# Performance work log

Hardware: AMD Instinct MI355X
Metric: run time of the kernel (lower is better)

The kernel has to match this reference:

```python
import jax, jax.numpy as jnp
import numpy as np

D_MODEL = 1024
N_HEAD = 16
D_HEAD = 64
BSZ = 2
QLEN = 2048
LOCAL_SIZE = 1000
LN_EPS = 1e-5


def setup_inputs() -> dict:
    key = jax.random.key(0)
    ks = jax.random.split(key, 8)
    z1ss = jax.random.normal(ks[0], (BSZ, D_MODEL, QLEN), jnp.float32)
    pos_emb = jax.random.normal(ks[1], (1, D_MODEL, QLEN), jnp.float32)
    u1ss = jax.random.normal(ks[2], (BSZ, 3 * N_HEAD * D_HEAD, QLEN), jnp.float32) * 0.05
    W_qkv = jax.random.normal(ks[3], (3 * N_HEAD * D_HEAD, D_MODEL), jnp.float32) * 0.02
    W_r = jax.random.normal(ks[4], (N_HEAD * D_HEAD, D_MODEL), jnp.float32) * 0.02
    r_w_bias = jax.random.uniform(ks[5], (N_HEAD, D_HEAD), jnp.float32, -0.05, 0.05)
    r_r_bias = jax.random.uniform(ks[6], (N_HEAD, D_HEAD), jnp.float32, -0.05, 0.05)
    W_o = jax.random.normal(ks[7], (D_MODEL, N_HEAD * D_HEAD), jnp.float32) * 0.02
    b_o = jnp.zeros((D_MODEL,), jnp.float32)
    return dict(z1ss=z1ss, pos_emb=pos_emb, u1ss=u1ss, W_qkv=W_qkv, W_r=W_r,
                r_w_bias=r_w_bias, r_r_bias=r_r_bias, W_o=W_o, b_o=b_o)


def _rel_shift(x):
    # Transformer-XL relative-shift trick: pad one column on the left, reshape,
    # drop first row, reshape back. x: [b, n, qlen, klen]
    b, n, q, k = x.shape
    xp = jnp.pad(x, ((0, 0), (0, 0), (0, 0), (1, 0)))
    return xp.reshape(b, n, k + 1, q)[:, :, 1:, :].reshape(b, n, q, k)


def reference(z1ss, pos_emb, u1ss, W_qkv, W_r, r_w_bias, r_r_bias, W_o, b_o):
    bsz, d_model, qlen = z1ss.shape
    n_head, d_head = r_w_bias.shape
    klen = qlen  # mems=None -> mlen=0
    scale = 1.0 / (d_head ** 0.5)

    # Conv1d(kernel_size=1, bias=False) == per-position linear
    w_heads = jnp.einsum('od,bdq->boq', W_qkv, z1ss) + u1ss        # [b, 3*n*d, q]
    r_head_k = jnp.einsum('od,dq->oq', W_r, pos_emb[0]).reshape(n_head, d_head, klen)

    q_h, k_h, v_h = jnp.split(w_heads, 3, axis=1)
    q_h = q_h.reshape(bsz, n_head, d_head, qlen)
    k_h = k_h.reshape(bsz, n_head, d_head, klen)
    v_h = v_h.reshape(bsz, n_head, d_head, klen)

    AC = jnp.einsum('bndi,bndj->bnij', q_h + r_w_bias[:, :, None], k_h)
    BD = _rel_shift(jnp.einsum('bndi,ndj->bnij', q_h + r_r_bias[:, :, None], r_head_k))
    attn_score = (AC + BD) * scale                                  # [b, n, q, k]

    # causal + local-window mask (mlen=0)
    ones = jnp.ones((qlen, klen), dtype=bool)
    mask = jnp.triu(ones, 1) | jnp.tril(ones, -LOCAL_SIZE)
    attn_score = jnp.where(mask[None, None], -jnp.inf, attn_score)

    attn_prob = jax.nn.softmax(attn_score, axis=-1)
    attn_vec = jnp.einsum('bnij,bndj->bndi', attn_prob, v_h)
    attn_vec = attn_vec.reshape(bsz, n_head * d_head, qlen)

    attn_out = jnp.einsum('od,bdq->boq', W_o, attn_vec) + b_o[None, :, None]

    # post-LN residual: layer_norm over d_model (no affine params)
    x = (attn_out + z1ss).transpose(0, 2, 1)                        # [b, q, d]
    mu = x.mean(-1, keepdims=True)
    var = ((x - mu) ** 2).mean(-1, keepdims=True)
    x = (x - mu) / jnp.sqrt(var + LN_EPS)
    return x.transpose(0, 2, 1)                                     # [b, d, q]
```

## Files before the change

kernel.cpp:

```cpp
#include <hip/hip_runtime.h>
#include <hip/hip_bf16.h>

#define D_MODEL 1024
#define N_HEAD 16
#define BSZ 2
#define QLEN 2048
#define LOCAL_SIZE 1000
#define QKV3 (3 * N_HEAD * 64)

typedef __hip_bfloat16 bf16;
typedef short bf16x8 __attribute__((ext_vector_type(8)));
typedef float f32x4 __attribute__((ext_vector_type(4)));

static __device__ __forceinline__ float b2f(bf16 x) { return __bfloat162float(x); }
static __device__ __forceinline__ float bits2f(unsigned short u) {
    return __uint_as_float(((unsigned int)u) << 16);
}
static __device__ __forceinline__ unsigned short f2bs(float x) {
    __hip_bfloat16 h = __float2bfloat16(x);
    return *(unsigned short*)&h;
}

static __device__ __forceinline__ int rmode(int m, int fl) { return (m == 2) ? fl : m; }
static __device__ __forceinline__ float ldm(const void* p, size_t i, int isf) {
    return isf ? ((const float*)p)[i] : b2f(((const bf16*)p)[i]);
}
static __device__ __forceinline__ float4 ld4(const void* p, size_t i, int isf) {
    if (isf) return ((const float4*)p)[i >> 2];
    ushort4 u = ((const ushort4*)p)[i >> 2];
    float4 f;
    f.x = bits2f(u.x); f.y = bits2f(u.y); f.z = bits2f(u.z); f.w = bits2f(u.w);
    return f;
}
static __device__ __forceinline__ ushort4 cvt4(float4 f) {
    ushort4 u;
    u.x = f2bs(f.x); u.y = f2bs(f.y); u.z = f2bs(f.z); u.w = f2bs(f.w);
    return u;
}

__global__ void detect_kernel(const unsigned short* __restrict__ w, int* __restrict__ flag)
{
    if (threadIdx.x == 0 && blockIdx.x == 0) {
        int good = 0;
        for (int i = 0; i < 256; ++i) {
            float v = bits2f(w[i]);
            if (v == v && fabsf(v) < 8.0f) ++good;
        }
        *flag = (good >= 240) ? 0 : 1;
    }
}

__global__ __launch_bounds__(256)
void transpose_cvt(const void* __restrict__ in, bf16* __restrict__ outp,
                   int rows, int cols, size_t sIn, size_t sOut,
                   const int* __restrict__ flag)
{
    const int fl = *flag;
    const int b  = blockIdx.z;
    const int c0 = blockIdx.x * 32;
    const int r0 = blockIdx.y * 32;
    const int tx = threadIdx.x & 31, ty = threadIdx.x >> 5;
    __shared__ float T[32][33];
#pragma unroll
    for (int r = 0; r < 4; ++r) {
        int rr = r0 + ty + r * 8;
        T[ty + r * 8][tx] = ldm(in, (size_t)b * sIn + (size_t)rr * cols + c0 + tx, fl);
    }
    __syncthreads();
#pragma unroll
    for (int r = 0; r < 4; ++r) {
        int cc = c0 + ty + r * 8;
        outp[(size_t)b * sOut + (size_t)cc * rows + r0 + tx] =
            __float2bfloat16(T[tx][ty + r * 8]);
    }
}

__global__ __launch_bounds__(256)
void gemm_bf16(const void* __restrict__ A, int mA, size_t sAb,
               const void* __restrict__ B, int mB, size_t sBb,
               void* __restrict__ C, int c_is_bf16, size_t sCb,
               const void* __restrict__ addm, int mAdd, size_t sAddb,
               const void* __restrict__ bias, int mBias,
               int M, int N, int K, const int* __restrict__ flag)
{
    const int fl = *flag;
    const int fA = rmode(mA, fl), fB = rmode(mB, fl);
    const int fAdd = rmode(mAdd, fl), fBias = rmode(mBias, fl);

    const int bz = blockIdx.z;
    const int n0 = blockIdx.x * 128;
    const int m0 = blockIdx.y * 128;
    const int tid = threadIdx.x;
    const int wave = tid >> 6, lane = tid & 63;
    const int quad = lane >> 4, l15 = lane & 15;
    const int wm = (wave >> 1) * 64, wn = (wave & 1) * 64;

    __shared__ unsigned short A_s[128][40];
    __shared__ unsigned short B_s[128][40];

    const int r0c = tid >> 2,         c0c = tid & 3;
    const int r1c = (tid + 256) >> 2, c1c = tid & 3;

    const size_t aOff = (size_t)bz * sAb;
    const size_t bOff = (size_t)bz * sBb;
    const bf16*  Ah = (const bf16*)A;
    const float* Af = (const float*)A;
    const bf16*  Bh = (const bf16*)B;
    const float* Bf = (const float*)B;

    uint4 pa[4], pb[4];

#define LOAD_OP(p, fX, Xh, Xf, xOff, R0, C0, R1, C1, base, k0)                          \
    do {                                                                                \
        if (!fX) {                                                                      \
            p[0] = *(const uint4*)(Xh + xOff + (size_t)(base + R0) * K + (k0) + C0 * 8);\
            p[1] = *(const uint4*)(Xh + xOff + (size_t)(base + R1) * K + (k0) + C1 * 8);\
        } else {                                                                        \
            const float* q0 = Xf + xOff + (size_t)(base + R0) * K + (k0) + C0 * 8;      \
            const float* q1 = Xf + xOff + (size_t)(base + R1) * K + (k0) + C1 * 8;      \
            p[0] = *(const uint4*)q0; p[1] = *(const uint4*)(q0 + 4);                   \
            p[2] = *(const uint4*)q1; p[3] = *(const uint4*)(q1 + 4);                   \
        }                                                                               \
    } while (0)

#define WRITE_OP(p, fX, S, R0, C0, R1, C1)                                              \
    do {                                                                                \
        if (!fX) {                                                                      \
            *(uint4*)&S[R0][C0 * 8] = p[0];                                             \
            *(uint4*)&S[R1][C1 * 8] = p[1];                                             \
        } else {                                                                        \
            float4 f0 = *(float4*)&p[0], f1 = *(float4*)&p[1];                          \
            float4 f2 = *(float4*)&p[2], f3 = *(float4*)&p[3];                          \
            *(ushort4*)&S[R0][C0 * 8]     = cvt4(f0);                                   \
            *(ushort4*)&S[R0][C0 * 8 + 4] = cvt4(f1);                                   \
            *(ushort4*)&S[R1][C1 * 8]     = cvt4(f2);                                   \
            *(ushort4*)&S[R1][C1 * 8 + 4] = cvt4(f3);                                   \
        }                                                                               \
    } while (0)

    f32x4 acc[4][4];
#pragma unroll
    for (int i = 0; i < 4; ++i)
#pragma unroll
        for (int j = 0; j < 4; ++j) acc[i][j] = (f32x4){0.f, 0.f, 0.f, 0.f};

    LOAD_OP(pa, fA, Ah, Af, aOff, r0c, c0c, r1c, c1c, m0, 0);
    LOAD_OP(pb, fB, Bh, Bf, bOff, r0c, c0c, r1c, c1c, n0, 0);

    for (int k0 = 0; k0 < K; k0 += 32) {
        WRITE_OP(pa, fA, A_s, r0c, c0c, r1c, c1c);
        WRITE_OP(pb, fB, B_s, r0c, c0c, r1c, c1c);
        __syncthreads();

        const int kn = k0 + 32;
        if (kn < K) {
            LOAD_OP(pa, fA, Ah, Af, aOff, r0c, c0c, r1c, c1c, m0, kn);
            LOAD_OP(pb, fB, Bh, Bf, bOff, r0c, c0c, r1c, c1c, n0, kn);
        }

        bf16x8 a[4], bb[4];
#pragma unroll
        for (int i = 0; i < 4; ++i)
            a[i] = *(const bf16x8*)&A_s[wm + i * 16 + l15][quad * 8];
#pragma unroll
        for (int j = 0; j < 4; ++j)
            bb[j] = *(const bf16x8*)&B_s[wn + j * 16 + l15][quad * 8];
#pragma unroll
        for (int i = 0; i < 4; ++i)
#pragma unroll
            for (int j = 0; j < 4; ++j)
                acc[i][j] = __builtin_amdgcn_mfma_f32_16x16x32_bf16(a[i], bb[j], acc[i][j], 0, 0, 0);
        __syncthreads();
    }
#undef LOAD_OP
#undef WRITE_OP

    const size_t cb = (size_t)bz * sCb;
#pragma unroll
    for (int i = 0; i < 4; ++i) {
#pragma unroll
        for (int j = 0; j < 4; ++j) {
            int n = n0 + wn + j * 16 + l15;
#pragma unroll
            for (int r = 0; r < 4; ++r) {
                int m = m0 + wm + i * 16 + quad * 4 + r;
                float v = acc[i][j][r];
                if (addm) v += ldm(addm, (size_t)bz * sAddb + (size_t)m * N + n, fAdd);
                if (bias) v += ldm(bias, (size_t)n, fBias);
                size_t ci = cb + (size_t)m * N + n;
                if (c_is_bf16) ((bf16*)C)[ci] = __float2bfloat16(v);
                else           ((float*)C)[ci] = v;
            }
        }
    }
}

__global__ __launch_bounds__(256)
void gemm_tn(const void* __restrict__ A, int mA, size_t sAb,
             const void* __restrict__ Bsrc, int mB, int bTrans, int ldB, size_t sBb,
             void* __restrict__ C, int c_is_bf16, size_t sCb,
             const void* __restrict__ addm, int mAdd, int addT, size_t sAddb,
             const void* __restrict__ bias, int mBias,
             int M, int N, int K, const int* __restrict__ flag)
{
    const int fl = *flag;
    const int fA = rmode(mA, fl), fB = rmode(mB, fl);
    const int fAdd = rmode(mAdd, fl), fBias = rmode(mBias, fl);

    const int bz = blockIdx.z;
    const int n0 = blockIdx.x * 128;
    const int m0 = blockIdx.y * 128;
    const int tid = threadIdx.x;
    const int wave = tid >> 6, lane = tid & 63;
    const int quad = lane >> 4, l15 = lane & 15;
    const int wm = (wave >> 1) * 64, wn = (wave & 1) * 64;

    __shared__ unsigned short A_s[128][40];
    __shared__ unsigned short B_s[128][40];

    const size_t aBase = (size_t)bz * sAb;
    const size_t bBase = (size_t)bz * sBb;

    f32x4 acc[4][4];
#pragma unroll
    for (int i = 0; i < 4; ++i)
#pragma unroll
        for (int j = 0; j < 4; ++j) acc[i][j] = (f32x4){0.f, 0.f, 0.f, 0.f};

    for (int k0 = 0; k0 < K; k0 += 32) {
#pragma unroll
        for (int g = 0; g < 4; ++g) {
            int c = tid + g * 256;
            int m = c >> 3, kc = (c & 7) * 4;
            float4 f = ld4(A, aBase + (size_t)(m0 + m) * K + k0 + kc, fA);
            *(ushort4*)&A_s[m][kc] = cvt4(f);
        }
        if (!bTrans) {
#pragma unroll
            for (int g = 0; g < 4; ++g) {
                int c = tid + g * 256;
                int n = c >> 3, kc = (c & 7) * 4;
                float4 f = ld4(Bsrc, bBase + (size_t)(n0 + n) * ldB + k0 + kc, fB);
                *(ushort4*)&B_s[n][kc] = cvt4(f);
            }
        } else {
#pragma unroll
            for (int g = 0; g < 4; ++g) {
                int c = tid + g * 256;
                int k = c >> 5, nc = (c & 31) * 4;
                float4 f = ld4(Bsrc, bBase + (size_t)(k0 + k) * ldB + n0 + nc, fB);
                ushort4 u = cvt4(f);
                B_s[nc + 0][k] = u.x;
                B_s[nc + 1][k] = u.y;
                B_s[nc + 2][k] = u.z;
                B_s[nc + 3][k] = u.w;
            }
        }
        __syncthreads();

        bf16x8 a[4], bb[4];
#pragma unroll
        for (int i = 0; i < 4; ++i)
            a[i] = *(const bf16x8*)&A_s[wm + i * 16 + l15][quad * 8];
#pragma unroll
        for (int j = 0; j < 4; ++j)
            bb[j] = *(const bf16x8*)&B_s[wn + j * 16 + l15][quad * 8];
#pragma unroll
        for (int i = 0; i < 4; ++i)
#pragma unroll
            for (int j = 0; j < 4; ++j)
                acc[i][j] = __builtin_amdgcn_mfma_f32_16x16x32_bf16(a[i], bb[j], acc[i][j], 0, 0, 0);
        __syncthreads();
    }

    const size_t cb = (size_t)bz * sCb;
#pragma unroll
    for (int i = 0; i < 4; ++i) {
#pragma unroll
        for (int j = 0; j < 4; ++j) {
            int n = n0 + wn + j * 16 + l15;
#pragma unroll
            for (int r = 0; r < 4; ++r) {
                int m = m0 + wm + i * 16 + quad * 4 + r;
                float v = acc[i][j][r];
                if (addm) {
                    size_t ai = (size_t)bz * sAddb +
                                (addT ? ((size_t)n * M + m) : ((size_t)m * N + n));
                    v += ldm(addm, ai, fAdd);
                }
                if (bias) v += ldm(bias, (size_t)n, fBias);
                size_t ci = cb + (size_t)m * N + n;
                if (c_is_bf16) ((bf16*)C)[ci] = __float2bfloat16(v);
                else           ((float*)C)[ci] = v;
            }
        }
    }
}

__global__ __launch_bounds__(256)
void attn_mfma(const bf16* __restrict__ wh,
               const bf16* __restrict__ rhk,
               const void* __restrict__ rwb,
               const void* __restrict__ rrb,
               bf16* __restrict__ av_out,
               const int* __restrict__ flag)
{
    const int fl = *flag;
    const int it = blockIdx.x, h = blockIdx.y, b = blockIdx.z;
    const int i0 = it * 64;
    const int tid = threadIdx.x;
    const int wave = tid >> 6, lane = tid & 63;
    const int quad = lane >> 4, l15 = lane & 15;
    const int hw = h * 64;

    __shared__ __align__(16) unsigned short sm[18944];
    unsigned short* KtPs = sm;
    unsigned short* Vs   = sm + 4608;
    unsigned short* Rt   = sm + 9216;
    unsigned short* Gs   = sm + 9216;
    unsigned short* Qrw  = sm;
    unsigned short* Qrr  = sm + 4608;

    const bf16* whb = wh + (size_t)b * QKV3 * QLEN;
    const int d_t = tid & 63;
    const int dv0 = tid >> 3, jv0 = (tid & 7) * 8;
    const int dv1 = (tid + 256) >> 3;

    int lo = i0 - (LOCAL_SIZE - 1);
    if (lo < 0) lo = 0;
    const int jt_lo = lo >> 6;
    const int j0_lo = jt_lo * 64;

    {
        float brw = ldm(rwb, hw + d_t, fl);
        float brr = ldm(rrb, hw + d_t, fl);
        const bf16* qrow = whb + (size_t)(hw + d_t) * QLEN + i0;
        uint4 qv0 = *(const uint4*)(qrow + wave * 8);
        uint4 qv1 = *(const uint4*)(qrow + (4 + wave) * 8);
        const int pbase0 = j0_lo - i0 + QLEN - 64;
        const bf16* rrow = rhk + (size_t)(hw + d_t) * QLEN;
        uint4 rv0i = *(const uint4*)(rrow + pbase0 + wave * 8);
        uint4 rv1i = *(const uint4*)(rrow + pbase0 + (4 + wave) * 8);

        unsigned short u8[8];
        *(uint4*)u8 = qv0;
#pragma unroll
        for (int u = 0; u < 8; ++u) {
            float q = bits2f(u8[u]);
            Qrw[(wave * 8 + u) * 72 + d_t] = f2bs(q + brw);
            Qrr[(wave * 8 + u) * 72 + d_t] = f2bs(q + brr);
        }
        *(uint4*)u8 = qv1;
#pragma unroll
        for (int u = 0; u < 8; ++u) {
            float q = bits2f(u8[u]);
            Qrw[((4 + wave) * 8 + u) * 72 + d_t] = f2bs(q + brw);
            Qrr[((4 + wave) * 8 + u) * 72 + d_t] = f2bs(q + brr);
        }
        *(uint4*)u8 = rv0i;
#pragma unroll
        for (int u = 0; u < 8; ++u) Rt[(wave * 8 + u) * 72 + d_t] = u8[u];
        *(uint4*)u8 = rv1i;
#pragma unroll
        for (int u = 0; u < 8; ++u) Rt[((4 + wave) * 8 + u) * 72 + d_t] = u8[u];
    }

    uint4 kv0, kv1, vv0, vv1, rv0, rv1;
    {
        const int j0 = j0_lo;
        const bf16* krow = whb + (size_t)(1024 + hw + d_t) * QLEN + j0;
        kv0 = *(const uint4*)(krow + wave * 8);
        kv1 = *(const uint4*)(krow + (4 + wave) * 8);
        vv0 = *(const uint4*)(whb + (size_t)(2048 + hw + dv0) * QLEN + j0 + jv0);
        vv1 = *(const uint4*)(whb + (size_t)(2048 + hw + dv1) * QLEN + j0 + jv0);
        const int pn = j0 - i0 + QLEN;
        const bf16* rrow = rhk + (size_t)(hw + d_t) * QLEN;
        int p0 = pn + wave * 8;
        if (p0 + 7 < QLEN) rv0 = *(const uint4*)(rrow + p0);
        else {
            unsigned short u8[8];
#pragma unroll
            for (int u = 0; u < 8; ++u)
                u8[u] = (p0 + u < QLEN) ? *(const unsigned short*)(rrow + p0 + u) : 0;
            rv0 = *(uint4*)u8;
        }
        int p1 = pn + (4 + wave) * 8;
        if (p1 + 7 < QLEN) rv1 = *(const uint4*)(rrow + p1);
        else {
            unsigned short u8[8];
#pragma unroll
            for (int u = 0; u < 8; ++u)
                u8[u] = (p1 + u < QLEN) ? *(const unsigned short*)(rrow + p1 + u) : 0;
            rv1 = *(uint4*)u8;
        }
    }
    __syncthreads();

    const int qrow_off = (wave * 16 + l15) * 72 + quad * 8;
    bf16x8 qw0 = *(const bf16x8*)&Qrw[qrow_off];
    bf16x8 qw1 = *(const bf16x8*)&Qrw[qrow_off + 32];
    bf16x8 qr0 = *(const bf16x8*)&Qrr[qrow_off];
    bf16x8 qr1 = *(const bf16x8*)&Qrr[qrow_off + 32];

    f32x4 g_acc[8];
#pragma unroll
    for (int nt = 0; nt < 4; ++nt) {
        f32x4 g = (f32x4){0.f, 0.f, 0.f, 0.f};
        int ro = (nt * 16 + l15) * 72 + quad * 8;
        bf16x8 b0 = *(const bf16x8*)&Rt[ro];
        bf16x8 b1 = *(const bf16x8*)&Rt[ro + 32];
        g = __builtin_amdgcn_mfma_f32_16x16x32_bf16(qr0, b0, g, 0, 0, 0);
        g = __builtin_amdgcn_mfma_f32_16x16x32_bf16(qr1, b1, g, 0, 0, 0);
        g_acc[nt] = g;
    }

    float l_r[4] = {0.f, 0.f, 0.f, 0.f};
    f32x4 o_acc[4];
#pragma unroll
    for (int dj = 0; dj < 4; ++dj) o_acc[dj] = (f32x4){0.f, 0.f, 0.f, 0.f};

    for (int jt = jt_lo; jt <= it; ++jt) {
        const int j0 = jt * 64;
        __syncthreads();

        {
            unsigned short u8[8];
            *(uint4*)u8 = kv0;
#pragma unroll
            for (int u = 0; u < 8; ++u) KtPs[(wave * 8 + u) * 72 + d_t] = u8[u];
            *(uint4*)u8 = kv1;
#pragma unroll
            for (int u = 0; u < 8; ++u) KtPs[((4 + wave) * 8 + u) * 72 + d_t] = u8[u];
            *(uint4*)&Vs[dv0 * 72 + jv0] = vv0;
            *(uint4*)&Vs[dv1 * 72 + jv0] = vv1;
            *(uint4*)u8 = rv0;
#pragma unroll
            for (int u = 0; u < 8; ++u) Rt[(wave * 8 + u) * 72 + d_t] = u8[u];
            *(uint4*)u8 = rv1;
#pragma unroll
            for (int u = 0; u < 8; ++u) Rt[((4 + wave) * 8 + u) * 72 + d_t] = u8[u];
        }

        if (jt < it) {
            const int j0n = j0 + 64;
            const bf16* krow = whb + (size_t)(1024 + hw + d_t) * QLEN + j0n;
            kv0 = *(const uint4*)(krow + wave * 8);
            kv1 = *(const uint4*)(krow + (4 + wave) * 8);
            vv0 = *(const uint4*)(whb + (size_t)(2048 + hw + dv0) * QLEN + j0n + jv0);
            vv1 = *(const uint4*)(whb + (size_t)(2048 + hw + dv1) * QLEN + j0n + jv0);
            const int pn = j0n - i0 + QLEN;
            const bf16* rrow = rhk + (size_t)(hw + d_t) * QLEN;
            int p0 = pn + wave * 8;
            if (p0 + 7 < QLEN) rv0 = *(const uint4*)(rrow + p0);
            else {
                unsigned short u8[8];
#pragma unroll
                for (int u = 0; u < 8; ++u)
                    u8[u] = (p0 + u < QLEN) ? *(const unsigned short*)(rrow + p0 + u) : 0;
                rv0 = *(uint4*)u8;
            }
            int p1 = pn + (4 + wave) * 8;
            if (p1 + 7 < QLEN) rv1 = *(const uint4*)(rrow + p1);
            else {
                unsigned short u8[8];
#pragma unroll
                for (int u = 0; u < 8; ++u)
                    u8[u] = (p1 + u < QLEN) ? *(const unsigned short*)(rrow + p1 + u) : 0;
                rv1 = *(uint4*)u8;
            }
        }
        __syncthreads();

        f32x4 s_acc[4];
#pragma unroll
        for (int nj = 0; nj < 4; ++nj) {
            s_acc[nj] = (f32x4){0.f, 0.f, 0.f, 0.f};
            int ko = (nj * 16 + l15) * 72 + quad * 8;
            bf16x8 b0 = *(const bf16x8*)&KtPs[ko];
            bf16x8 b1 = *(const bf16x8*)&KtPs[ko + 32];
            s_acc[nj] = __builtin_amdgcn_mfma_f32_16x16x32_bf16(qw0, b0, s_acc[nj], 0, 0, 0);
            s_acc[nj] = __builtin_amdgcn_mfma_f32_16x16x32_bf16(qw1, b1, s_acc[nj], 0, 0, 0);
        }
#pragma unroll
        for (int nt = 0; nt < 4; ++nt) {
            f32x4 g = (f32x4){0.f, 0.f, 0.f, 0.f};
            int ro = (nt * 16 + l15) * 72 + quad * 8;
            bf16x8 b0 = *(const bf16x8*)&Rt[ro];
            bf16x8 b1 = *(const bf16x8*)&Rt[ro + 32];
            g = __builtin_amdgcn_mfma_f32_16x16x32_bf16(qr0, b0, g, 0, 0, 0);
            g = __builtin_amdgcn_mfma_f32_16x16x32_bf16(qr1, b1, g, 0, 0, 0);
            g_acc[4 + nt] = g;
        }
        __syncthreads();

#pragma unroll
        for (int nt = 0; nt < 8; ++nt) {
            ushort4 u;
            u.x = f2bs(g_acc[nt][0]);
            u.y = f2bs(g_acc[nt][1]);
            u.z = f2bs(g_acc[nt][2]);
            u.w = f2bs(g_acc[nt][3]);
            *(ushort4*)&Gs[(nt * 16 + l15) * 76 + wave * 16 + quad * 4] = u;
        }

        float rs[4] = {0.f, 0.f, 0.f, 0.f};
#pragma unroll
        for (int nj = 0; nj < 4; ++nj) {
#pragma unroll
            for (int r = 0; r < 4; ++r) {
                int i_loc = wave * 16 + quad * 4 + r;
                int j_loc = nj * 16 + l15;
                int t = j_loc - i_loc + 63;
                float bd = bits2f(Gs[t * 76 + i_loc]);
                int diff = (i0 + i_loc) - (j0 + j_loc);
                float p = 0.f;
                if (diff >= 0 && diff < LOCAL_SIZE)
                    p = __expf((s_acc[nj][r] + bd) * 0.125f);
                KtPs[i_loc * 72 + j_loc] = f2bs(p);
                rs[r] += p;
            }
        }
#pragma unroll
        for (int r = 0; r < 4; ++r) {
            float v = rs[r];
            v += __shfl_xor(v, 1);
            v += __shfl_xor(v, 2);
            v += __shfl_xor(v, 4);
            v += __shfl_xor(v, 8);
            l_r[r] += v;
        }

        {
            int po = (wave * 16 + l15) * 72 + quad * 8;
            bf16x8 pa0 = *(const bf16x8*)&KtPs[po];
            bf16x8 pa1 = *(const bf16x8*)&KtPs[po + 32];
#pragma unroll
            for (int dj = 0; dj < 4; ++dj) {
                int vo = (dj * 16 + l15) * 72 + quad * 8;
                bf16x8 b0 = *(const bf16x8*)&Vs[vo];
                bf16x8 b1 = *(const bf16x8*)&Vs[vo + 32];
                o_acc[dj] = __builtin_amdgcn_mfma_f32_16x16x32_bf16(pa0, b0, o_acc[dj], 0, 0, 0);
                o_acc[dj] = __builtin_amdgcn_mfma_f32_16x16x32_bf16(pa1, b1, o_acc[dj], 0, 0, 0);
            }
        }

#pragma unroll
        for (int nt = 0; nt < 4; ++nt) g_acc[nt] = g_acc[nt + 4];
    }

#pragma unroll
    for (int r = 0; r < 4; ++r) {
        float inv = 1.f / l_r[r];
        int q = i0 + wave * 16 + quad * 4 + r;
        bf16* orow = av_out + ((size_t)b * QLEN + q) * D_MODEL + hw;
#pragma unroll
        for (int dj = 0; dj < 4; ++dj)
            orow[dj * 16 + l15] = __float2bfloat16(o_acc[dj][r] * inv);
    }
}

__global__ __launch_bounds__(256)
void ln_kernel(float* __restrict__ yt)
{
    const int b = blockIdx.y, q = blockIdx.x;
    float* row = yt + ((size_t)b * QLEN + q) * D_MODEL;
    const int t = threadIdx.x;
    float4 v = ((float4*)row)[t];
    float s  = v.x + v.y + v.z + v.w;
    float ss = v.x * v.x + v.y * v.y + v.z * v.z + v.w * v.w;
#pragma unroll
    for (int off = 32; off; off >>= 1) {
        s  += __shfl_down(s, off);
        ss += __shfl_down(ss, off);
    }
    __shared__ float sw[4], ssw[4];
    const int w = t >> 6;
    if ((t & 63) == 0) { sw[w] = s; ssw[w] = ss; }
    __syncthreads();
    float S  = sw[0] + sw[1] + sw[2] + sw[3];
    float SS = ssw[0] + ssw[1] + ssw[2] + ssw[3];
    float mu  = S / D_MODEL;
    float var = SS / D_MODEL - mu * mu;
    float rs  = rsqrtf(var + 1e-5f);
    v.x = (v.x - mu) * rs; v.y = (v.y - mu) * rs;
    v.z = (v.z - mu) * rs; v.w = (v.w - mu) * rs;
    ((float4*)row)[t] = v;
}

__global__ __launch_bounds__(256)
void transpose_out(const float* __restrict__ yt, void* __restrict__ out,
                   const int* __restrict__ flag)
{
    const int fl = *flag;
    const int b  = blockIdx.z;
    const int q0 = blockIdx.x * 32;
    const int o0 = blockIdx.y * 32;
    const int tx = threadIdx.x & 31, ty = threadIdx.x >> 5;
    __shared__ float T[32][33];
#pragma unroll
    for (int r = 0; r < 4; ++r) {
        int q = q0 + ty + r * 8;
        T[ty + r * 8][tx] = yt[((size_t)b * QLEN + q) * D_MODEL + o0 + tx];
    }
    __syncthreads();
#pragma unroll
    for (int r = 0; r < 4; ++r) {
        int o = o0 + ty + r * 8;
        size_t oi = ((size_t)b * D_MODEL + o) * QLEN + q0 + tx;
        float v = T[tx][ty + r * 8];
        if (fl) ((float*)out)[oi] = v;
        else    ((bf16*)out)[oi] = __float2bfloat16(v);
    }
}

extern "C" void kernel_launch(void* const* d_in, const int* in_sizes, int n_in,
                              void* d_out, int out_size, void* d_ws, size_t ws_size,
                              hipStream_t stream)
{
    const void* z1ss = d_in[0];
    const void* pos  = d_in[1];
    const void* u1ss = d_in[2];
    const void* Wqkv = d_in[3];
    const void* Wr   = d_in[4];
    const void* rwb  = d_in[5];
    const void* rrb  = d_in[6];
    const void* Wo   = d_in[7];
    const void* bo   = d_in[8];

    const size_t whE  = (size_t)BSZ * QKV3 * QLEN;
    const size_t rhkE = (size_t)D_MODEL * QLEN;
    const size_t avE  = (size_t)BSZ * QLEN * D_MODEL;
    const size_t ztE  = avE;

    char* ws = (char*)d_ws;
    bf16* wh   = (bf16*)ws;
    bf16* rhk  = wh + whE;
    bf16* avec = rhk + rhkE;
    bf16* post = avec;
    size_t baseB = (whE + rhkE + avE) * sizeof(bf16);
    const bool big = ws_size >= baseB + ztE * sizeof(bf16) + 16;
    bf16* zt = (bf16*)(ws + baseB);
    int* flag = (int*)(ws + baseB + (big ? ztE * sizeof(bf16) : 0));
    float* yt = (float*)ws;

    detect_kernel<<<1, 64, 0, stream>>>((const unsigned short*)Wqkv, flag);

    if (big) {
        transpose_cvt<<<dim3(QLEN / 32, D_MODEL / 32, BSZ), 256, 0, stream>>>(
            z1ss, zt, D_MODEL, QLEN, (size_t)D_MODEL * QLEN, (size_t)QLEN * D_MODEL, flag);
        transpose_cvt<<<dim3(QLEN / 32, D_MODEL / 32, 1), 256, 0, stream>>>(
            pos, post, D_MODEL, QLEN, 0, 0, flag);

        gemm_bf16<<<dim3(2048 / 128, 3072 / 128, BSZ), 256, 0, stream>>>(
            Wqkv, 2, 0,
            zt, 0, (size_t)QLEN * D_MODEL,
            wh, 1, (size_t)QKV3 * QLEN,
            u1ss, 2, (size_t)QKV3 * QLEN,
            nullptr, 0,
            QKV3, QLEN, D_MODEL, flag);

        gemm_bf16<<<dim3(2048 / 128, 1024 / 128, 1), 256, 0, stream>>>(
            Wr, 2, 0,
            post, 0, 0,
            rhk, 1, 0,
            nullptr, 0, 0,
            nullptr, 0,
            D_MODEL, QLEN, D_MODEL, flag);

        attn_mfma<<<dim3(QLEN / 64, N_HEAD, BSZ), 256, 0, stream>>>(
            wh, rhk, rwb, rrb, avec, flag);

        gemm_bf16<<<dim3(1024 / 128, 2048 / 128, BSZ), 256, 0, stream>>>(
            avec, 0, (size_t)QLEN * D_MODEL,
            Wo, 2, 0,
            yt, 0, (size_t)QLEN * D_MODEL,
            zt, 0, (size_t)QLEN * D_MODEL,
            bo, 2,
            QLEN, D_MODEL, D_MODEL, flag);
    } else {
        gemm_tn<<<dim3(2048 / 128, 3072 / 128, BSZ), 256, 0, stream>>>(
            Wqkv, 2, 0,
            z1ss, 2, 1, QLEN, (size_t)D_MODEL * QLEN,
            wh, 1, (size_t)QKV3 * QLEN,
            u1ss, 2, 0, (size_t)QKV3 * QLEN,
            nullptr, 0,
            QKV3, QLEN, D_MODEL, flag);
        gemm_tn<<<dim3(2048 / 128, 1024 / 128, 1), 256, 0, stream>>>(
            Wr, 2, 0,
            pos, 2, 1, QLEN, 0,
            rhk, 1, 0,
            nullptr, 0, 0, 0,
            nullptr, 0,
            D_MODEL, QLEN, D_MODEL, flag);
        attn_mfma<<<dim3(QLEN / 64, N_HEAD, BSZ), 256, 0, stream>>>(
            wh, rhk, rwb, rrb, avec, flag);
        gemm_tn<<<dim3(1024 / 128, 2048 / 128, BSZ), 256, 0, stream>>>(
            avec, 0, (size_t)QLEN * D_MODEL,
            Wo, 2, 0, D_MODEL, 0,
            yt, 0, (size_t)QLEN * D_MODEL,
            z1ss, 2, 1, (size_t)D_MODEL * QLEN,
            bo, 2,
            QLEN, D_MODEL, D_MODEL, flag);
    }

    ln_kernel<<<dim3(QLEN, BSZ), 256, 0, stream>>>(yt);

    transpose_out<<<dim3(QLEN / 32, D_MODEL / 32, BSZ), 256, 0, stream>>>(yt, d_out, flag);
}
```

Baseline: 476.7 us.

## Pre-convert weights to bf16 and use global_load_lds double-buffered GEMM

Adds a workspace tier that first converts the three weight matrices to bf16, then runs a new GEMM kernel. That kernel streams A/B tiles from global memory straight into LDS with global_load_lds and double-buffers them, so the GEMM no longer needs mixed-precision load handling or register staging. The point is to cut load overhead and overlap the next tile's loads with MFMA work. In exchange it needs more workspace, adds three conversion launches, and falls back to the old path when the workspace is too small.

```diff
diff --git a/kernel.cpp b/kernel.cpp
--- a/kernel.cpp
+++ b/kernel.cpp
@@ -38,6 +38,13 @@
     return u;
 }
 
+static __device__ __forceinline__ void glds16(const bf16* g, unsigned short* l) {
+    __builtin_amdgcn_global_load_lds(
+        (const __attribute__((address_space(1))) void*)g,
+        (__attribute__((address_space(3))) void*)l,
+        16, 0, 0);
+}
+
 __global__ void detect_kernel(const unsigned short* __restrict__ w, int* __restrict__ flag)
 {
     if (threadIdx.x == 0 && blockIdx.x == 0) {
@@ -47,6 +54,22 @@
             if (v == v && fabsf(v) < 8.0f) ++good;
         }
         *flag = (good >= 240) ? 0 : 1;
+    }
+}
+
+__global__ __launch_bounds__(256)
+void convw(const void* __restrict__ in, bf16* __restrict__ out,
+           const int* __restrict__ flag)
+{
+    const int fl = *flag;
+    size_t i = ((size_t)blockIdx.x * 256 + threadIdx.x) * 8;
+    if (fl) {
+        float4 a = ((const float4*)in)[i / 4];
+        float4 b = ((const float4*)in)[i / 4 + 1];
+        *(ushort4*)((unsigned short*)out + i)     = cvt4(a);
+        *(ushort4*)((unsigned short*)out + i + 4) = cvt4(b);
+    } else {
+        *(uint4*)((unsigned short*)out + i) = ((const uint4*)in)[i / 8];
     }
 }
 
@@ -72,6 +95,90 @@
         int cc = c0 + ty + r * 8;
         outp[(size_t)b * sOut + (size_t)cc * rows + r0 + tx] =
             __float2bfloat16(T[tx][ty + r * 8]);
+    }
+}
+
+__global__ __launch_bounds__(256)
+void gemm_glds(const bf16* __restrict__ A, size_t sAb,
+               const bf16* __restrict__ B, size_t sBb,
+               void* __restrict__ C, int c_is_bf16, size_t sCb,
+               const void* __restrict__ addm, int mAdd, size_t sAddb,
+               const void* __restrict__ bias, int mBias,
+               int M, int N, int K, const int* __restrict__ flag)
+{
+    const int fl = *flag;
+    const int fAdd = rmode(mAdd, fl), fBias = rmode(mBias, fl);
+
+    const int bz = blockIdx.z;
+    const int n0 = blockIdx.x * 128;
+    const int m0 = blockIdx.y * 128;
+    const int tid = threadIdx.x;
+    const int wave = tid >> 6, lane = tid & 63;
+    const int quad = lane >> 4, l15 = lane & 15;
+    const int wm = (wave >> 1) * 64, wn = (wave & 1) * 64;
+
+    __shared__ __align__(16) unsigned short A_s[2][128 * 32];
+    __shared__ __align__(16) unsigned short B_s[2][128 * 32];
+
+    const int srow = wave * 32 + (lane >> 2);
+    const int scol = (lane & 3) * 8;
+    const bf16* Ag = A + (size_t)bz * sAb + (size_t)(m0 + srow) * K + scol;
+    const bf16* Bg = B + (size_t)bz * sBb + (size_t)(n0 + srow) * K + scol;
+    const int sbase = wave * 1024;
+
+    f32x4 acc[4][4];
+#pragma unroll
+    for (int i = 0; i < 4; ++i)
+#pragma unroll
+        for (int j = 0; j < 4; ++j) acc[i][j] = (f32x4){0.f, 0.f, 0.f, 0.f};
+
+    glds16(Ag,                   &A_s[0][sbase]);
+    glds16(Ag + (size_t)16 * K,  &A_s[0][sbase + 512]);
+    glds16(Bg,                   &B_s[0][sbase]);
+    glds16(Bg + (size_t)16 * K,  &B_s[0][sbase + 512]);
+
+    int cur = 0;
+    for (int k0 = 0; k0 < K; k0 += 32) {
+        __syncthreads();
+        if (k0 + 32 < K) {
+            const int kn = k0 + 32;
+            glds16(Ag + kn,                  &A_s[cur ^ 1][sbase]);
+            glds16(Ag + (size_t)16 * K + kn, &A_s[cur ^ 1][sbase + 512]);
+            glds16(Bg + kn,                  &B_s[cur ^ 1][sbase]);
+            glds16(Bg + (size_t)16 * K + kn, &B_s[cur ^ 1][sbase + 512]);
+        }
+        bf16x8 a[4], bb[4];
+#pragma unroll
+        for (int i = 0; i < 4; ++i)
+            a[i] = *(const bf16x8*)&A_s[cur][(wm + i * 16 + l15) * 32 + quad * 8];
+#pragma unroll
+        for (int j = 0; j < 4; ++j)
+            bb[j] = *(const bf16x8*)&B_s[cur][(wn + j * 16 + l15) * 32 + quad * 8];
+#pragma unroll
+        for (int i = 0; i < 4; ++i)
+#pragma unroll
+            for (int j = 0; j < 4; ++j)
+                acc[i][j] = __builtin_amdgcn_mfma_f32_16x16x32_bf16(a[i], bb[j], acc[i][j], 0, 0, 0);
+        cur ^= 1;
+    }
+
+    const size_t cb = (size_t)bz * sCb;
+#pragma unroll
+    for (int i = 0; i < 4; ++i) {
+#pragma unroll
+        for (int j = 0; j < 4; ++j) {
+            int n = n0 + wn + j * 16 + l15;
+#pragma unroll
+            for (int r = 0; r < 4; ++r) {
+                int m = m0 + wm + i * 16 + quad * 4 + r;
+                float v = acc[i][j][r];
+                if (addm) v += ldm(addm, (size_t)bz * sAddb + (size_t)m * N + n, fAdd);
+                if (bias) v += ldm(bias, (size_t)n, fBias);
+                size_t ci = cb + (size_t)m * N + n;
+                if (c_is_bf16) ((bf16*)C)[ci] = __float2bfloat16(v);
+                else           ((float*)C)[ci] = v;
+            }
+        }
     }
 }
 
@@ -631,6 +738,9 @@
     const size_t rhkE = (size_t)D_MODEL * QLEN;
     const size_t avE  = (size_t)BSZ * QLEN * D_MODEL;
     const size_t ztE  = avE;
+    const size_t wqE  = (size_t)QKV3 * D_MODEL;
+    const size_t wrE  = (size_t)D_MODEL * D_MODEL;
+    const size_t woE  = wrE;
 
     char* ws = (char*)d_ws;
     bf16* wh   = (bf16*)ws;
@@ -638,14 +748,59 @@
     bf16* avec = rhk + rhkE;
     bf16* post = avec;
     size_t baseB = (whE + rhkE + avE) * sizeof(bf16);
-    const bool big = ws_size >= baseB + ztE * sizeof(bf16) + 16;
-    bf16* zt = (bf16*)(ws + baseB);
-    int* flag = (int*)(ws + baseB + (big ? ztE * sizeof(bf16) : 0));
+    bf16* zt  = (bf16*)(ws + baseB);
+    bf16* wqb = zt + ztE;
+    bf16* wrb = wqb + wqE;
+    bf16* wob = wrb + wrE;
     float* yt = (float*)ws;
 
+    const size_t t2B = baseB + ztE * sizeof(bf16) + 16;
+    const size_t t1B = baseB + (ztE + wqE + wrE + woE) * sizeof(bf16) + 16;
+    const int tier = (ws_size >= t1B) ? 1 : (ws_size >= t2B) ? 2 : 3;
+
+    int* flag = (tier == 1) ? (int*)(wob + woE)
+              : (tier == 2) ? (int*)(wqb)
+                            : (int*)(ws + baseB);
+
     detect_kernel<<<1, 64, 0, stream>>>((const unsigned short*)Wqkv, flag);
 
-    if (big) {
+    if (tier == 1) {
+        convw<<<dim3(wqE / 2048), 256, 0, stream>>>(Wqkv, wqb, flag);
+        convw<<<dim3(wrE / 2048), 256, 0, stream>>>(Wr,   wrb, flag);
+        convw<<<dim3(woE / 2048), 256, 0, stream>>>(Wo,   wob, flag);
+
+        transpose_cvt<<<dim3(QLEN / 32, D_MODEL / 32, BSZ), 256, 0, stream>>>(
+            z1ss, zt, D_MODEL, QLEN, (size_t)D_MODEL * QLEN, (size_t)QLEN * D_MODEL, flag);
+        transpose_cvt<<<dim3(QLEN / 32, D_MODEL / 32, 1), 256, 0, stream>>>(
+            pos, post, D_MODEL, QLEN, 0, 0, flag);
+
+        gemm_glds<<<dim3(2048 / 128, 3072 / 128, BSZ), 256, 0, stream>>>(
+            wqb, 0,
+            zt, (size_t)QLEN * D_MODEL,
+            wh, 1, (size_t)QKV3 * QLEN,
+            u1ss, 2, (size_t)QKV3 * QLEN,
+            nullptr, 0,
+            QKV3, QLEN, D_MODEL, flag);
+
+        gemm_glds<<<dim3(2048 / 128, 1024 / 128, 1), 256, 0, stream>>>(
+            wrb, 0,
+            post, 0,
+            rhk, 1, 0,
+            nullptr, 0, 0,
+            nullptr, 0,
+            D_MODEL, QLEN, D_MODEL, flag);
+
+        attn_mfma<<<dim3(QLEN / 64, N_HEAD, BSZ), 256, 0, stream>>>(
+            wh, rhk, rwb, rrb, avec, flag);
+
+        gemm_glds<<<dim3(1024 / 128, 2048 / 128, BSZ), 256, 0, stream>>>(
+            avec, (size_t)QLEN * D_MODEL,
+            wob, 0,
+            yt, 0, (size_t)QLEN * D_MODEL,
+            zt, 0, (size_t)QLEN * D_MODEL,
+            bo, 2,
+            QLEN, D_MODEL, D_MODEL, flag);
+    } else if (tier == 2) {
         transpose_cvt<<<dim3(QLEN / 32, D_MODEL / 32, BSZ), 256, 0, stream>>>(
             z1ss, zt, D_MODEL, QLEN, (size_t)D_MODEL * QLEN, (size_t)QLEN * D_MODEL, flag);
         transpose_cvt<<<dim3(QLEN / 32, D_MODEL / 32, 1), 256, 0, stream>>>(
```

Result: faster. 406.7 us (-14.7%).
